# Kernel optimization log

Measured on AMD Instinct MI355X. Metric: run time of the kernel, lower is better.

Reference implementation:

```python
import jax, jax.numpy as jnp
import numpy as np

B, N, D, E = 8, 512, 256, 16384  # batch, num_nodes, hidden_dim, num_edges


def setup_inputs() -> dict:
    key = jax.random.key(0)
    kf, ke, k1, k2, k3, k4 = jax.random.split(key, 6)
    features = jax.random.normal(kf, (B, N, D), dtype=jnp.float32)
    edge_index = jax.random.randint(ke, (2, E), 0, N, dtype=jnp.int64)
    # weight_net: Linear(2D -> D), ReLU, Linear(D -> 1), Sigmoid
    s1 = 1.0 / np.sqrt(2 * D)
    s2 = 1.0 / np.sqrt(D)
    W1 = jax.random.uniform(k1, (2 * D, D), jnp.float32, -s1, s1)
    b1 = jax.random.uniform(k2, (D,), jnp.float32, -s1, s1)
    W2 = jax.random.uniform(k3, (D, 1), jnp.float32, -s2, s2)
    b2 = jax.random.uniform(k4, (1,), jnp.float32, -s2, s2)
    return {"features": features, "W1": W1, "b1": b1, "W2": W2, "b2": b2,
            "edge_index": edge_index}


def reference(features, W1, b1, W2, b2, edge_index):
    src, dst = edge_index[0], edge_index[1]            # [E], [E]
    fi = features[:, src]                              # [B, E, D]
    fj = features[:, dst]                              # [B, E, D]
    pair = jnp.concatenate([fi, fj], axis=-1)          # [B, E, 2D]
    h = jax.nn.relu(jnp.einsum('bef,fh->beh', pair, W1) + b1)   # [B, E, D]
    s = jax.nn.sigmoid(jnp.einsum('beh,ho->beo', h, W2) + b2)[..., 0]  # [B, E]
    bsz, n = features.shape[0], features.shape[1]
    weights = jnp.zeros((bsz, n, n), features.dtype).at[:, src, dst].set(s)
    return weights
```

## Files before the change

### kernel.cpp

```cpp
#include <hip/hip_runtime.h>
#include <cstdint>

#define B_ 8
#define N_ 512
#define D_ 256
#define E_ 16384

#define SBK 264
#define NBLK 512

using bf16x8 = __attribute__((ext_vector_type(8))) short;
using f32x4  = __attribute__((ext_vector_type(4))) float;

__device__ inline unsigned short f2bf(float f) {
    union { float f; unsigned u; } v; v.f = f;
    unsigned u = v.u;
    return (unsigned short)((u + 0x7fffu + ((u >> 16) & 1u)) >> 16);
}

__device__ inline float dot8nb(uint4 qu, uint4 qv, const float* w2p) {
    unsigned us[4] = {qu.x, qu.y, qu.z, qu.w};
    unsigned vs[4] = {qv.x, qv.y, qv.z, qv.w};
    float p = 0.f;
#pragma unroll
    for (int j = 0; j < 4; j++) {
        float ulo = __uint_as_float(us[j] << 16);
        float uhi = __uint_as_float(us[j] & 0xffff0000u);
        float vlo = __uint_as_float(vs[j] << 16);
        float vhi = __uint_as_float(vs[j] & 0xffff0000u);
        float hlo = fmaxf(ulo + vlo, 0.f);
        float hhi = fmaxf(uhi + vhi, 0.f);
        p = fmaf(hlo, w2p[2 * j],     p);
        p = fmaf(hhi, w2p[2 * j + 1], p);
    }
    return p;
}

__device__ inline void grid_barrier(int* cnt, int* flag) {
    __syncthreads();
    if (threadIdx.x == 0) {
        asm volatile("s_waitcnt vmcnt(0) lgkmcnt(0)" ::: "memory");
        int prev = __hip_atomic_fetch_add(cnt, 1, __ATOMIC_RELAXED,
                                          __HIP_MEMORY_SCOPE_AGENT);
        if (prev == NBLK - 1) {
            __hip_atomic_store(flag, 1, __ATOMIC_RELAXED, __HIP_MEMORY_SCOPE_AGENT);
        } else {
            for (int it = 0; it < (1 << 17); ++it) {
                if (__hip_atomic_load(flag, __ATOMIC_RELAXED,
                                      __HIP_MEMORY_SCOPE_AGENT) != 0) break;
                if ((it & 63) == 63 &&
                    __hip_atomic_fetch_add(flag, 0, __ATOMIC_RELAXED,
                                           __HIP_MEMORY_SCOPE_AGENT) != 0) break;
                __builtin_amdgcn_s_sleep(2);
            }
        }
        asm volatile("" ::: "memory");
    }
    __syncthreads();
}

__global__ __launch_bounds__(256, 4)
void fused(const float* __restrict__ feat, const float* __restrict__ W1,
           const float* __restrict__ b1,   const float* __restrict__ W2,
           const float* __restrict__ b2,   const int* __restrict__ eidx,
           unsigned short* __restrict__ P, int* __restrict__ gBar,
           float* __restrict__ out)
{
    __shared__ __align__(16) char smem[35840];
    unsigned short* sB = (unsigned short*)smem;
    int* sES = (int*)(smem + 33792);
    int* sED = sES + 256;

    const int bid = blockIdx.x, t = threadIdx.x;
    const int b   = bid & 7;
    const int loc = bid >> 3;
    const int m0  = b * 512 + (loc >> 3) * 64;
    const int bn  = loc & 7;
    const int n0  = bn * 64;

    sES[t] = eidx[loc * 256 + t];
    sED[t] = eidx[E_ + loc * 256 + t];

    {
        float4 z = make_float4(0.f, 0.f, 0.f, 0.f);
        float4* oz = (float4*)(out + ((size_t)b * 512 + (size_t)loc * 8) * 512) + t;
#pragma unroll
        for (int i = 0; i < 4; i++) oz[i * 256] = z;
    }

    {
        const int h = bn >> 2, c0 = (bn & 3) * 64;
        const int nn = t & 63, kg = t >> 6;
        const float* Wp = W1 + ((size_t)(h * 256 + kg * 64)) * 256 + c0 + nn;
        unsigned short* dstp = sB + nn * SBK + kg * 64;
#pragma unroll
        for (int o = 0; o < 8; o++) {
            union { bf16x8 v; unsigned short s[8]; } u;
#pragma unroll
            for (int j = 0; j < 8; j++)
                u.s[j] = f2bf(Wp[(size_t)(o * 8 + j) * 256]);
            *(bf16x8*)(dstp + o * 8) = u.v;
        }
    }
    __syncthreads();

    const int wave = t >> 6, lane = t & 63, l15 = lane & 15, quad = lane >> 4;
    {
        const float* pAw = feat + (size_t)(m0 + wave * 16 + l15) * 256 + quad * 8;
        f32x4 acc[4];
#pragma unroll
        for (int cn = 0; cn < 4; cn++) acc[cn] = (f32x4){0.f, 0.f, 0.f, 0.f};
#pragma unroll
        for (int ks = 0; ks < 8; ks++) {
            float4 lo = *(const float4*)(pAw + ks * 32);
            float4 hi = *(const float4*)(pAw + ks * 32 + 4);
            union { bf16x8 v; unsigned short s[8]; } u;
            u.s[0] = f2bf(lo.x); u.s[1] = f2bf(lo.y); u.s[2] = f2bf(lo.z); u.s[3] = f2bf(lo.w);
            u.s[4] = f2bf(hi.x); u.s[5] = f2bf(hi.y); u.s[6] = f2bf(hi.z); u.s[7] = f2bf(hi.w);
            bf16x8 af = u.v;
#pragma unroll
            for (int cn = 0; cn < 4; cn++) {
                bf16x8 bfr = *(const bf16x8*)(sB + (cn * 16 + l15) * SBK + ks * 32 + quad * 8);
                acc[cn] = __builtin_amdgcn_mfma_f32_16x16x32_bf16(af, bfr, acc[cn], 0, 0, 0);
            }
        }
#pragma unroll
        for (int cn = 0; cn < 4; cn++) {
            int col = n0 + cn * 16 + l15;
            float bias = (col < 256) ? b1[col] : 0.f;
#pragma unroll
            for (int r = 0; r < 4; r++) {
                int row = m0 + wave * 16 + quad * 4 + r;
                P[(size_t)row * 512 + col] = f2bf(acc[cn][r] + bias);
            }
        }
    }

    grid_barrier(gBar, gBar + 32);

    {
        const int g = lane >> 4, w = lane & 15;
        const int wid = wave * 4 + g;

        float w2r[16];
#pragma unroll
        for (int j = 0; j < 4; j++)
            *(float4*)(w2r + 4 * j) = *(const float4*)(W2 + w * 16 + 4 * j);
        const float b2v = b2[0];

        const unsigned short* Pb = P + (size_t)b * 512 * 512;
        float* outb = out + (size_t)b * 512 * 512;

        int e = wid;
        int s0 = sES[e], d0 = sED[e];
        const unsigned short* pu = Pb + (size_t)s0 * 512 + w * 16;
        const unsigned short* pv = Pb + (size_t)d0 * 512 + 256 + w * 16;
        uint4 u00 = *(const uint4*)pu, u01 = *(const uint4*)(pu + 8);
        uint4 v00 = *(const uint4*)pv, v01 = *(const uint4*)(pv + 8);

#pragma unroll 1
        for (int i = 0; i < 16; i++) {
            int en = e + 16;
            int s1 = 0, d1 = 0;
            uint4 u10 = {}, u11 = {}, v10 = {}, v11 = {};
            if (i < 15) {
                s1 = sES[en]; d1 = sED[en];
                const unsigned short* qu = Pb + (size_t)s1 * 512 + w * 16;
                const unsigned short* qv = Pb + (size_t)d1 * 512 + 256 + w * 16;
                u10 = *(const uint4*)qu; u11 = *(const uint4*)(qu + 8);
                v10 = *(const uint4*)qv; v11 = *(const uint4*)(qv + 8);
            }
            float p = dot8nb(u00, v00, w2r) + dot8nb(u01, v01, w2r + 8);
            p += __shfl_xor(p, 1);
            p += __shfl_xor(p, 2);
            p += __shfl_xor(p, 4);
            p += __shfl_xor(p, 8);
            if (w == 0)
                outb[(size_t)s0 * 512 + d0] = 1.0f / (1.0f + __expf(-(p + b2v)));
            s0 = s1; d0 = d1;
            u00 = u10; u01 = u11; v00 = v10; v01 = v11;
            e = en;
        }
    }
}

extern "C" void kernel_launch(void* const* d_in, const int* in_sizes, int n_in,
                              void* d_out, int out_size, void* d_ws, size_t ws_size,
                              hipStream_t stream) {
    const float* feat = (const float*)d_in[0];
    const float* W1   = (const float*)d_in[1];
    const float* b1   = (const float*)d_in[2];
    const float* W2   = (const float*)d_in[3];
    const float* b2   = (const float*)d_in[4];
    const int*   eidx = (const int*)d_in[5];
    float* out = (float*)d_out;

    int* gBar = (int*)d_ws;
    unsigned short* P = (unsigned short*)((char*)d_ws + 4096);

    hipMemsetAsync(d_ws, 0, 256, stream);
    fused<<<dim3(NBLK), dim3(256), 0, stream>>>(feat, W1, b1, W2, b2, eidx,
                                                P, gBar, out);
}
```

Before: 92.05 us.

## Split fused kernel at grid barrier into separate GEMM and edge kernels

Replaces the single persistent kernel and its atomic spin grid barrier with two kernel launches: a node-projection GEMM and an edge scoring kernel. Each kernel now uses 1024 blocks with smaller tiles (32 output columns per GEMM block, 128 edges per edge block). The edge kernel prefetches four edges at a time instead of a one-deep software pipeline. This removes the spin-barrier and the workspace memset, at the cost of an extra launch boundary and of staging the projected features through global memory between launches.

```diff
diff --git a/kernel.cpp b/kernel.cpp
--- a/kernel.cpp
+++ b/kernel.cpp
@@ -7,7 +7,7 @@
 #define E_ 16384
 
 #define SBK 264
-#define NBLK 512
+#define EPB 128
 
 using bf16x8 = __attribute__((ext_vector_type(8))) short;
 using f32x4  = __attribute__((ext_vector_type(4))) float;
@@ -36,65 +36,27 @@
     return p;
 }
 
-__device__ inline void grid_barrier(int* cnt, int* flag) {
-    __syncthreads();
-    if (threadIdx.x == 0) {
-        asm volatile("s_waitcnt vmcnt(0) lgkmcnt(0)" ::: "memory");
-        int prev = __hip_atomic_fetch_add(cnt, 1, __ATOMIC_RELAXED,
-                                          __HIP_MEMORY_SCOPE_AGENT);
-        if (prev == NBLK - 1) {
-            __hip_atomic_store(flag, 1, __ATOMIC_RELAXED, __HIP_MEMORY_SCOPE_AGENT);
-        } else {
-            for (int it = 0; it < (1 << 17); ++it) {
-                if (__hip_atomic_load(flag, __ATOMIC_RELAXED,
-                                      __HIP_MEMORY_SCOPE_AGENT) != 0) break;
-                if ((it & 63) == 63 &&
-                    __hip_atomic_fetch_add(flag, 0, __ATOMIC_RELAXED,
-                                           __HIP_MEMORY_SCOPE_AGENT) != 0) break;
-                __builtin_amdgcn_s_sleep(2);
-            }
-        }
-        asm volatile("" ::: "memory");
-    }
-    __syncthreads();
-}
-
 __global__ __launch_bounds__(256, 4)
-void fused(const float* __restrict__ feat, const float* __restrict__ W1,
-           const float* __restrict__ b1,   const float* __restrict__ W2,
-           const float* __restrict__ b2,   const int* __restrict__ eidx,
-           unsigned short* __restrict__ P, int* __restrict__ gBar,
-           float* __restrict__ out)
+void gemm_k(const float* __restrict__ feat, const float* __restrict__ W1,
+            const float* __restrict__ b1,   unsigned short* __restrict__ P,
+            float* __restrict__ out)
 {
-    __shared__ __align__(16) char smem[35840];
-    unsigned short* sB = (unsigned short*)smem;
-    int* sES = (int*)(smem + 33792);
-    int* sED = sES + 256;
+    __shared__ __align__(16) unsigned short sB[32 * SBK];
 
     const int bid = blockIdx.x, t = threadIdx.x;
     const int b   = bid & 7;
     const int loc = bid >> 3;
-    const int m0  = b * 512 + (loc >> 3) * 64;
-    const int bn  = loc & 7;
-    const int n0  = bn * 64;
-
-    sES[t] = eidx[loc * 256 + t];
-    sED[t] = eidx[E_ + loc * 256 + t];
+    const int m0  = b * 512 + (loc >> 4) * 64;
+    const int bn  = loc & 15;
+    const int n0  = bn * 32;
 
     {
-        float4 z = make_float4(0.f, 0.f, 0.f, 0.f);
-        float4* oz = (float4*)(out + ((size_t)b * 512 + (size_t)loc * 8) * 512) + t;
+        const int h = bn >> 3, c0 = (bn & 7) * 32;
+        const int col = t & 31, kg = t >> 5;
+        const float* Wp = W1 + ((size_t)(h * 256 + kg * 32)) * 256 + c0 + col;
+        unsigned short* dstp = sB + col * SBK + kg * 32;
 #pragma unroll
-        for (int i = 0; i < 4; i++) oz[i * 256] = z;
-    }
-
-    {
-        const int h = bn >> 2, c0 = (bn & 3) * 64;
-        const int nn = t & 63, kg = t >> 6;
-        const float* Wp = W1 + ((size_t)(h * 256 + kg * 64)) * 256 + c0 + nn;
-        unsigned short* dstp = sB + nn * SBK + kg * 64;
-#pragma unroll
-        for (int o = 0; o < 8; o++) {
+        for (int o = 0; o < 4; o++) {
             union { bf16x8 v; unsigned short s[8]; } u;
 #pragma unroll
             for (int j = 0; j < 8; j++)
@@ -102,14 +64,20 @@
             *(bf16x8*)(dstp + o * 8) = u.v;
         }
     }
+
+    {
+        float4 z = make_float4(0.f, 0.f, 0.f, 0.f);
+        float4* oz = (float4*)(out + ((size_t)b * 512 + (size_t)loc * 4) * 512) + t;
+        oz[0] = z; oz[256] = z;
+    }
     __syncthreads();
 
     const int wave = t >> 6, lane = t & 63, l15 = lane & 15, quad = lane >> 4;
     {
         const float* pAw = feat + (size_t)(m0 + wave * 16 + l15) * 256 + quad * 8;
-        f32x4 acc[4];
+        f32x4 acc[2];
 #pragma unroll
-        for (int cn = 0; cn < 4; cn++) acc[cn] = (f32x4){0.f, 0.f, 0.f, 0.f};
+        for (int cn = 0; cn < 2; cn++) acc[cn] = (f32x4){0.f, 0.f, 0.f, 0.f};
 #pragma unroll
         for (int ks = 0; ks < 8; ks++) {
             float4 lo = *(const float4*)(pAw + ks * 32);
@@ -119,13 +87,13 @@
             u.s[4] = f2bf(hi.x); u.s[5] = f2bf(hi.y); u.s[6] = f2bf(hi.z); u.s[7] = f2bf(hi.w);
             bf16x8 af = u.v;
 #pragma unroll
-            for (int cn = 0; cn < 4; cn++) {
+            for (int cn = 0; cn < 2; cn++) {
                 bf16x8 bfr = *(const bf16x8*)(sB + (cn * 16 + l15) * SBK + ks * 32 + quad * 8);
                 acc[cn] = __builtin_amdgcn_mfma_f32_16x16x32_bf16(af, bfr, acc[cn], 0, 0, 0);
             }
         }
 #pragma unroll
-        for (int cn = 0; cn < 4; cn++) {
+        for (int cn = 0; cn < 2; cn++) {
             int col = n0 + cn * 16 + l15;
             float bias = (col < 256) ? b1[col] : 0.f;
 #pragma unroll
@@ -135,52 +103,60 @@
             }
         }
     }
+}
 
-    grid_barrier(gBar, gBar + 32);
+__global__ __launch_bounds__(256, 4)
+void edge_k(const unsigned short* __restrict__ P, const float* __restrict__ W2,
+            const float* __restrict__ b2, const int* __restrict__ eidx,
+            float* __restrict__ out)
+{
+    __shared__ int sES[EPB], sED[EPB];
+    const int bid = blockIdx.x, t = threadIdx.x;
+    const int b = bid & 7, loc = bid >> 3;
 
-    {
-        const int g = lane >> 4, w = lane & 15;
-        const int wid = wave * 4 + g;
+    if (t < EPB) sES[t] = eidx[loc * EPB + t];
+    else         sED[t - EPB] = eidx[E_ + loc * EPB + (t - EPB)];
+    __syncthreads();
 
-        float w2r[16];
+    const int lane = t & 63, wave = t >> 6;
+    const int g = lane >> 4, w = lane & 15;
+    const int wid = wave * 4 + g;
+    const int e0 = wid * 8;
+
+    float w2r[16];
 #pragma unroll
-        for (int j = 0; j < 4; j++)
-            *(float4*)(w2r + 4 * j) = *(const float4*)(W2 + w * 16 + 4 * j);
-        const float b2v = b2[0];
+    for (int j = 0; j < 4; j++)
+        *(float4*)(w2r + 4 * j) = *(const float4*)(W2 + w * 16 + 4 * j);
+    const float b2v = b2[0];
 
-        const unsigned short* Pb = P + (size_t)b * 512 * 512;
-        float* outb = out + (size_t)b * 512 * 512;
+    const unsigned short* Pb = P + (size_t)b * 512 * 512;
+    float* outb = out + (size_t)b * 512 * 512;
 
-        int e = wid;
-        int s0 = sES[e], d0 = sED[e];
-        const unsigned short* pu = Pb + (size_t)s0 * 512 + w * 16;
-        const unsigned short* pv = Pb + (size_t)d0 * 512 + 256 + w * 16;
-        uint4 u00 = *(const uint4*)pu, u01 = *(const uint4*)(pu + 8);
-        uint4 v00 = *(const uint4*)pv, v01 = *(const uint4*)(pv + 8);
-
-#pragma unroll 1
-        for (int i = 0; i < 16; i++) {
-            int en = e + 16;
-            int s1 = 0, d1 = 0;
-            uint4 u10 = {}, u11 = {}, v10 = {}, v11 = {};
-            if (i < 15) {
-                s1 = sES[en]; d1 = sED[en];
-                const unsigned short* qu = Pb + (size_t)s1 * 512 + w * 16;
-                const unsigned short* qv = Pb + (size_t)d1 * 512 + 256 + w * 16;
-                u10 = *(const uint4*)qu; u11 = *(const uint4*)(qu + 8);
-                v10 = *(const uint4*)qv; v11 = *(const uint4*)(qv + 8);
-            }
-            float p = dot8nb(u00, v00, w2r) + dot8nb(u01, v01, w2r + 8);
-            p += __shfl_xor(p, 1);
-            p += __shfl_xor(p, 2);
-            p += __shfl_xor(p, 4);
-            p += __shfl_xor(p, 8);
-            if (w == 0)
-                outb[(size_t)s0 * 512 + d0] = 1.0f / (1.0f + __expf(-(p + b2v)));
-            s0 = s1; d0 = d1;
-            u00 = u10; u01 = u11; v00 = v10; v01 = v11;
-            e = en;
+    uint4 u0[4], u1[4], v0[4], v1[4];
+#pragma unroll
+    for (int i = 0; i < 4; i++) {
+        const unsigned short* pu = Pb + (size_t)sES[e0 + i] * 512 + w * 16;
+        const unsigned short* pv = Pb + (size_t)sED[e0 + i] * 512 + 256 + w * 16;
+        u0[i] = *(const uint4*)pu; u1[i] = *(const uint4*)(pu + 8);
+        v0[i] = *(const uint4*)pv; v1[i] = *(const uint4*)(pv + 8);
+    }
+#pragma unroll
+    for (int i = 0; i < 8; i++) {
+        const int sl = i & 3;
+        float p = dot8nb(u0[sl], v0[sl], w2r) + dot8nb(u1[sl], v1[sl], w2r + 8);
+        if (i < 4) {
+            const unsigned short* pu = Pb + (size_t)sES[e0 + i + 4] * 512 + w * 16;
+            const unsigned short* pv = Pb + (size_t)sED[e0 + i + 4] * 512 + 256 + w * 16;
+            u0[sl] = *(const uint4*)pu; u1[sl] = *(const uint4*)(pu + 8);
+            v0[sl] = *(const uint4*)pv; v1[sl] = *(const uint4*)(pv + 8);
         }
+        p += __shfl_xor(p, 1);
+        p += __shfl_xor(p, 2);
+        p += __shfl_xor(p, 4);
+        p += __shfl_xor(p, 8);
+        if (w == 0)
+            outb[(size_t)sES[e0 + i] * 512 + sED[e0 + i]] =
+                1.0f / (1.0f + __expf(-(p + b2v)));
     }
 }
 
@@ -195,10 +171,8 @@
     const int*   eidx = (const int*)d_in[5];
     float* out = (float*)d_out;
 
-    int* gBar = (int*)d_ws;
-    unsigned short* P = (unsigned short*)((char*)d_ws + 4096);
+    unsigned short* P = (unsigned short*)d_ws;
 
-    hipMemsetAsync(d_ws, 0, 256, stream);
-    fused<<<dim3(NBLK), dim3(256), 0, stream>>>(feat, W1, b1, W2, b2, eidx,
-                                                P, gBar, out);
+    gemm_k<<<dim3(1024), dim3(256), 0, stream>>>(feat, W1, b1, P, out);
+    edge_k<<<dim3(1024), dim3(256), 0, stream>>>(P, W2, b2, eidx, out);
 }
```

Result: faster. 86.72 us (-5.8%).
